# Kernel optimization log

Hardware: AMD Instinct MI355X
Metric: run time of the kernel (lower is better)

## Reference

```python
import math
import jax, jax.numpy as jnp
import numpy as np

SCALE = 64.0
MARGIN = 0.5
COS_M = math.cos(MARGIN)
SIN_M = math.sin(MARGIN)
TH = math.cos(math.pi - MARGIN)
MM = math.sin(math.pi - MARGIN) * MARGIN
EPS = 1e-12  # F.normalize default eps

B, D, C = 2048, 512, 100000


def setup_inputs() -> dict:
    key = jax.random.key(0)
    k1, k2, k3 = jax.random.split(key, 3)
    embeddings = jax.random.normal(k1, (B, D), dtype=jnp.float32)
    labels = jax.random.randint(k2, (B,), 0, C, dtype=jnp.int64)
    # xavier-uniform-like init for weight [C, D]
    limit = math.sqrt(6.0 / (C + D))
    weight = jax.random.uniform(k3, (C, D), dtype=jnp.float32, minval=-limit, maxval=limit)
    return {"embeddings": embeddings, "labels": labels, "weight": weight}


def _l2norm(x):
    n = jnp.linalg.norm(x, axis=-1, keepdims=True)
    return x / jnp.maximum(n, EPS)


def reference(embeddings, labels, weight):
    cosine = _l2norm(embeddings) @ _l2norm(weight).T  # [B, C]
    sine = jnp.sqrt(jnp.clip(1.0 - cosine * cosine, 0.0, None))
    phi = cosine * COS_M - sine * SIN_M
    phi = jnp.where(cosine > TH, phi, cosine - MM)
    # one-hot blend without materializing a separate one-hot tensor
    col = jnp.arange(cosine.shape[1])[None, :]
    is_target = col == labels[:, None]  # [B, C] bool
    logits = jnp.where(is_target, phi, cosine)
    return logits * SCALE
```

## Files before the change

### kernel.cpp

```cpp
#include <hip/hip_runtime.h>
#include <hip/hip_bf16.h>
#include <math.h>

constexpr int Bq = 2048;
constexpr int Dq = 512;
constexpr int Cq = 100000;
constexpr int NPAD = 100096;

constexpr float SCALE = 64.0f;
constexpr float COS_M = 0.8775825618903728f;
constexpr float SIN_M = 0.479425538604203f;
constexpr float THR   = -0.8775825618903728f;
constexpr float MM    = 0.2397127693021015f;

typedef __attribute__((ext_vector_type(8))) __bf16 bf16x8;
typedef __attribute__((ext_vector_type(4))) float f32x4;

typedef const __attribute__((address_space(1))) unsigned int guint;
typedef __attribute__((address_space(3))) unsigned int suint;

__device__ __forceinline__ void gload_lds16(const unsigned short* g, unsigned short* lds)
{
    __builtin_amdgcn_global_load_lds((guint*)g, (suint*)lds, 16, 0, 0);
}

__device__ __forceinline__ unsigned int pack_bf16x2(float lo, float hi)
{
    __hip_bfloat16 h0 = __float2bfloat16(lo);
    __hip_bfloat16 h1 = __float2bfloat16(hi);
    return ((unsigned int)(*(unsigned short*)&h1) << 16) |
           (unsigned int)(*(unsigned short*)&h0);
}

__global__ __launch_bounds__(256) void normalize_rows_kernel(
    const float* __restrict__ in, unsigned short* __restrict__ out, int nrows)
{
    const int w = threadIdx.x >> 6, lane = threadIdx.x & 63;
    const int row = blockIdx.x * 4 + w;
    float4 a = {0.f, 0.f, 0.f, 0.f}, b = a;
    if (row < nrows) {
        const float4* src = reinterpret_cast<const float4*>(in + (size_t)row * Dq);
        a = src[lane];
        b = src[lane + 64];
    }
    float ss = a.x * a.x + a.y * a.y + a.z * a.z + a.w * a.w
             + b.x * b.x + b.y * b.y + b.z * b.z + b.w * b.w;
    #pragma unroll
    for (int off = 32; off > 0; off >>= 1) ss += __shfl_down(ss, off);
    ss = __shfl(ss, 0);
    const float invn = 1.0f / fmaxf(sqrtf(ss), 1e-12f);

    uint2* out64 = reinterpret_cast<uint2*>(out + (size_t)row * Dq);
    uint2 pa, pb;
    pa.x = pack_bf16x2(a.x * invn, a.y * invn);
    pa.y = pack_bf16x2(a.z * invn, a.w * invn);
    pb.x = pack_bf16x2(b.x * invn, b.y * invn);
    pb.y = pack_bf16x2(b.z * invn, b.w * invn);
    out64[lane] = pa;
    out64[lane + 64] = pb;
}

__global__ __launch_bounds__(256, 2) void arc_gemm_kernel(
    const unsigned short* __restrict__ A,
    const unsigned short* __restrict__ Bn,
    const int* __restrict__ labels,
    float* __restrict__ out)
{
    extern __shared__ unsigned short lds[];

    const int cpx = (int)gridDim.x >> 3;
    const int bid = ((int)blockIdx.x & 7) * cpx + ((int)blockIdx.x >> 3);
    const int tm = bid & 15;
    const int tn = bid >> 4;
    const int m0 = tm * 128, n0 = tn * 128;

    const int t = threadIdx.x;
    const int w = t >> 6, lane = t & 63;
    const int wr = (w >> 1) * 64;
    const int wc = (w & 1) * 64;
    const int fr = lane & 15, kg = lane >> 4;
    const int s7 = fr & 7;
    const int c0 = (kg ^ s7) * 8;
    const int c1 = ((4 + kg) ^ s7) * 8;

    const int trow = t >> 3;
    const int tch = ((t & 7) ^ (trow & 7)) * 8;
    const unsigned short* gA = A  + (size_t)(m0 + trow) * Dq + tch;
    const unsigned short* gB = Bn + (size_t)(n0 + trow) * Dq + tch;
    const int dstA = trow * 64 + (t & 7) * 8;

#define STAGE_A(buf, s, kts) gload_lds16(gA + (size_t)(s) * 32 * Dq + (size_t)(kts) * 64, \
                                         &lds[(buf) * 16384 + (s) * 2048 + dstA])
#define STAGE_B(buf, s, kts) gload_lds16(gB + (size_t)(s) * 32 * Dq + (size_t)(kts) * 64, \
                                         &lds[(buf) * 16384 + 8192 + (s) * 2048 + dstA])
#define BARRIER() do { __builtin_amdgcn_sched_barrier(0); __builtin_amdgcn_s_barrier(); } while (0)

    f32x4 acc[4][4];
    #pragma unroll
    for (int i = 0; i < 4; ++i)
        #pragma unroll
        for (int j = 0; j < 4; ++j) acc[i][j] = {0.f, 0.f, 0.f, 0.f};

    STAGE_A(0, 0, 0); STAGE_A(0, 1, 0); STAGE_A(0, 2, 0); STAGE_A(0, 3, 0);
    STAGE_B(0, 0, 0); STAGE_B(0, 1, 0); STAGE_B(0, 2, 0); STAGE_B(0, 3, 0);
    STAGE_B(1, 0, 1); STAGE_B(1, 1, 1); STAGE_B(1, 2, 1); STAGE_B(1, 3, 1);
    STAGE_A(1, 0, 1); STAGE_A(1, 2, 1);
    asm volatile("s_waitcnt vmcnt(6)" ::: "memory");
    __builtin_amdgcn_s_barrier();

    const int arow = (wr + fr) * 64;
    const int brow = 8192 + (wc + fr) * 64;

#define LDA(q) do { \
    afr[0] = *reinterpret_cast<const bf16x8*>(&lds[cbo + arow + (q) * 1024 + c0]); \
    afr[1] = *reinterpret_cast<const bf16x8*>(&lds[cbo + arow + (q) * 1024 + c1]); \
} while (0)
#define LDB() do { \
    _Pragma("unroll") for (int ni = 0; ni < 4; ++ni) { \
        bfr[ni][0] = *reinterpret_cast<const bf16x8*>(&lds[cbo + brow + ni * 1024 + c0]); \
        bfr[ni][1] = *reinterpret_cast<const bf16x8*>(&lds[cbo + brow + ni * 1024 + c1]); } \
} while (0)
#define MFMA_QUAD(q) do { \
    __builtin_amdgcn_s_setprio(1); \
    _Pragma("unroll") for (int ks = 0; ks < 2; ++ks) \
    _Pragma("unroll") for (int ni = 0; ni < 4; ++ni) \
        acc[(q)][ni] = __builtin_amdgcn_mfma_f32_16x16x32_bf16( \
            bfr[ni][ks], afr[ks], acc[(q)][ni], 0, 0, 0); \
    __builtin_amdgcn_s_setprio(0); \
} while (0)

    #pragma unroll
    for (int kt = 0; kt < 8; ++kt) {
        const int cb = kt & 1, nb = cb ^ 1;
        const int cbo = cb * 16384;
        bf16x8 bfr[4][2];
        bf16x8 afr[2];
        LDB(); LDA(0);
        if (kt < 7) { STAGE_A(nb, 1, kt + 1); STAGE_A(nb, 3, kt + 1); }
        BARRIER();
        MFMA_QUAD(0);
        BARRIER();
        LDA(1);
        if (kt < 6) { STAGE_B(cb, 0, kt + 2); STAGE_B(cb, 1, kt + 2); }
        BARRIER();
        MFMA_QUAD(1);
        BARRIER();
        LDA(2);
        if (kt < 6) { STAGE_B(cb, 2, kt + 2); STAGE_B(cb, 3, kt + 2); }
        BARRIER();
        MFMA_QUAD(2);
        BARRIER();
        LDA(3);
        if (kt < 6) { STAGE_A(cb, 0, kt + 2); STAGE_A(cb, 2, kt + 2); }
        BARRIER();
        MFMA_QUAD(3);
        if (kt < 6) asm volatile("s_waitcnt vmcnt(6)" ::: "memory");
        else        asm volatile("s_waitcnt vmcnt(0)" ::: "memory");
        BARRIER();
    }

    float* lf = reinterpret_cast<float*>(lds);
    #pragma unroll
    for (int mi = 0; mi < 4; ++mi) {
        const int lrow = wr + mi * 16 + fr;
        const int lab = labels[m0 + lrow];
        #pragma unroll
        for (int ni = 0; ni < 4; ++ni) {
            const int col0 = wc + ni * 16 + kg * 4;
            const int gcol0 = n0 + col0;
            f32x4 v = acc[mi][ni];
            #pragma unroll
            for (int r = 0; r < 4; ++r) {
                if (gcol0 + r == lab) {
                    float c = v[r];
                    float sine = sqrtf(fmaxf(1.0f - c * c, 0.0f));
                    float phi = c * COS_M - sine * SIN_M;
                    v[r] = (c > THR) ? phi : (c - MM);
                }
            }
            v *= SCALE;
            *reinterpret_cast<f32x4*>(&lf[lrow * 132 + col0]) = v;
        }
    }
    __syncthreads();
    const int cc = lane & 31, rh = lane >> 5;
    #pragma unroll
    for (int s = 0; s < 16; ++s) {
        const int lrow = (w * 16 + s) * 2 + rh;
        f32x4 v = *reinterpret_cast<const f32x4*>(&lf[lrow * 132 + cc * 4]);
        const int gcol0 = n0 + cc * 4;
        if (gcol0 < Cq)
            __builtin_nontemporal_store(
                v, reinterpret_cast<f32x4*>(out + (size_t)(m0 + lrow) * Cq + gcol0));
    }
#undef STAGE_A
#undef STAGE_B
#undef BARRIER
#undef LDA
#undef LDB
#undef MFMA_QUAD
}

extern "C" void kernel_launch(void* const* d_in, const int* in_sizes, int n_in,
                              void* d_out, int out_size, void* d_ws, size_t ws_size,
                              hipStream_t stream)
{
    const float* emb    = (const float*)d_in[0];
    const int*   labels = (const int*)d_in[1];
    const float* weight = (const float*)d_in[2];
    float* out = (float*)d_out;

    unsigned short* Abf = (unsigned short*)d_ws;
    unsigned short* Bbf = Abf + (size_t)Bq * Dq;

    normalize_rows_kernel<<<Bq / 4, 256, 0, stream>>>(emb, Abf, Bq);
    normalize_rows_kernel<<<NPAD / 4, 256, 0, stream>>>(weight, Bbf, Cq);
    arc_gemm_kernel<<<16 * (NPAD / 128), 256, 67584, stream>>>(Abf, Bbf, labels, out);
}
```

Measured before the change: 325.6 us.

## Merge quad MFMA phases into two paired phases with fewer barriers

Restructures each K-step's inner schedule from four load/MFMA phases with eight barriers into two phases that each handle two A-quads, with four barriers. Two A fragments are loaded at once and their MFMAs are interleaved, which reduces barrier stalls and gives the MFMA units longer independent chains. In exchange, register pressure rises and the six global-to-LDS prefetches are grouped into one burst instead of being spread out, which may reduce latency hiding.

```diff
diff --git a/kernel.cpp b/kernel.cpp
--- a/kernel.cpp
+++ b/kernel.cpp
@@ -111,21 +111,23 @@
     const int arow = (wr + fr) * 64;
     const int brow = 8192 + (wc + fr) * 64;
 
-#define LDA(q) do { \
-    afr[0] = *reinterpret_cast<const bf16x8*>(&lds[cbo + arow + (q) * 1024 + c0]); \
-    afr[1] = *reinterpret_cast<const bf16x8*>(&lds[cbo + arow + (q) * 1024 + c1]); \
+#define LDAQ(dst, q) do { \
+    dst[0] = *reinterpret_cast<const bf16x8*>(&lds[cbo + arow + (q) * 1024 + c0]); \
+    dst[1] = *reinterpret_cast<const bf16x8*>(&lds[cbo + arow + (q) * 1024 + c1]); \
 } while (0)
 #define LDB() do { \
     _Pragma("unroll") for (int ni = 0; ni < 4; ++ni) { \
         bfr[ni][0] = *reinterpret_cast<const bf16x8*>(&lds[cbo + brow + ni * 1024 + c0]); \
         bfr[ni][1] = *reinterpret_cast<const bf16x8*>(&lds[cbo + brow + ni * 1024 + c1]); } \
 } while (0)
-#define MFMA_QUAD(q) do { \
+#define MFMA_PAIR(q0, a0, q1, a1) do { \
     __builtin_amdgcn_s_setprio(1); \
     _Pragma("unroll") for (int ks = 0; ks < 2; ++ks) \
-    _Pragma("unroll") for (int ni = 0; ni < 4; ++ni) \
-        acc[(q)][ni] = __builtin_amdgcn_mfma_f32_16x16x32_bf16( \
-            bfr[ni][ks], afr[ks], acc[(q)][ni], 0, 0, 0); \
+    _Pragma("unroll") for (int ni = 0; ni < 4; ++ni) { \
+        acc[(q0)][ni] = __builtin_amdgcn_mfma_f32_16x16x32_bf16( \
+            bfr[ni][ks], a0[ks], acc[(q0)][ni], 0, 0, 0); \
+        acc[(q1)][ni] = __builtin_amdgcn_mfma_f32_16x16x32_bf16( \
+            bfr[ni][ks], a1[ks], acc[(q1)][ni], 0, 0, 0); } \
     __builtin_amdgcn_s_setprio(0); \
 } while (0)
 
@@ -134,26 +136,20 @@
         const int cb = kt & 1, nb = cb ^ 1;
         const int cbo = cb * 16384;
         bf16x8 bfr[4][2];
-        bf16x8 afr[2];
-        LDB(); LDA(0);
+        bf16x8 af0[2], af1[2], af2[2], af3[2];
+        LDB(); LDAQ(af0, 0); LDAQ(af1, 1);
         if (kt < 7) { STAGE_A(nb, 1, kt + 1); STAGE_A(nb, 3, kt + 1); }
         BARRIER();
-        MFMA_QUAD(0);
-        BARRIER();
-        LDA(1);
-        if (kt < 6) { STAGE_B(cb, 0, kt + 2); STAGE_B(cb, 1, kt + 2); }
-        BARRIER();
-        MFMA_QUAD(1);
-        BARRIER();
-        LDA(2);
-        if (kt < 6) { STAGE_B(cb, 2, kt + 2); STAGE_B(cb, 3, kt + 2); }
-        BARRIER();
-        MFMA_QUAD(2);
-        BARRIER();
-        LDA(3);
-        if (kt < 6) { STAGE_A(cb, 0, kt + 2); STAGE_A(cb, 2, kt + 2); }
-        BARRIER();
-        MFMA_QUAD(3);
+        MFMA_PAIR(0, af0, 1, af1);
+        BARRIER();
+        LDAQ(af2, 2); LDAQ(af3, 3);
+        if (kt < 6) {
+            STAGE_B(cb, 0, kt + 2); STAGE_B(cb, 1, kt + 2);
+            STAGE_B(cb, 2, kt + 2); STAGE_B(cb, 3, kt + 2);
+            STAGE_A(cb, 0, kt + 2); STAGE_A(cb, 2, kt + 2);
+        }
+        BARRIER();
+        MFMA_PAIR(2, af2, 3, af3);
         if (kt < 6) asm volatile("s_waitcnt vmcnt(6)" ::: "memory");
         else        asm volatile("s_waitcnt vmcnt(0)" ::: "memory");
         BARRIER();
@@ -196,9 +192,9 @@
 #undef STAGE_A
 #undef STAGE_B
 #undef BARRIER
-#undef LDA
+#undef LDAQ
 #undef LDB
-#undef MFMA_QUAD
+#undef MFMA_PAIR
 }
 
 extern "C" void kernel_launch(void* const* d_in, const int* in_sizes, int n_in,
```

Result: no change. 325.2 us (-0.1%).
